# Performance work log

Measured on AMD Instinct MI355X. Metric: run time of the kernel, lower is better.

The kernel has to match this reference:

```python
import jax, jax.numpy as jnp
import numpy as np

N, D, H, O = 200000, 256, 256, 128


def _linear_params(key, fan_in, fan_out):
    # matches torch.nn.Linear default init: U(-1/sqrt(fan_in), 1/sqrt(fan_in))
    lim = 1.0 / np.sqrt(fan_in)
    kw, kb = jax.random.split(key)
    W = jax.random.uniform(kw, (fan_in, fan_out), minval=-lim, maxval=lim, dtype=jnp.float32)
    b = jax.random.uniform(kb, (fan_out,), minval=-lim, maxval=lim, dtype=jnp.float32)
    return W, b


def setup_inputs() -> dict:
    key = jax.random.key(0)
    ks = jax.random.split(key, 6)
    node_embeddings = jax.random.normal(ks[0], (N, D), dtype=jnp.float32)
    # adjacency_list keys: all < N so every key is 'valid'
    adj_keys = jax.random.randint(ks[1], (N,), 0, N, dtype=jnp.int64) if jax.config.jax_enable_x64 else jax.random.randint(ks[1], (N,), 0, N, dtype=jnp.int32)
    W1, b1 = _linear_params(ks[2], D, H)
    W2, b2 = _linear_params(ks[3], H, H)
    W3, b3 = _linear_params(ks[4], H, H)
    Wo, bo = _linear_params(ks[5], H, O)
    return {
        "node_embeddings": node_embeddings,
        "adj_keys": adj_keys,
        "W1": W1, "b1": b1,
        "W2": W2, "b2": b2,
        "W3": W3, "b3": b3,
        "Wo": Wo, "bo": bo,
    }


def reference(node_embeddings, adj_keys, W1, b1, W2, b2, W3, b3, Wo, bo):
    # --- aggregation path (faithful to the torch code's actual math) ---
    # All adj_keys are < N, so valid_indices == keys and the re-enumeration
    # `mapping` makes `indices` exactly arange(num_keys).
    indices = jnp.arange(adj_keys.shape[0])
    neighbors = node_embeddings[indices]              # [N, D] row gather
    # torch.mean(row, dim=0) on a 1-D row == scalar mean over features
    aggregated_embeddings = jnp.mean(neighbors, axis=1)  # [N]

    # --- dense 3-layer SAGE MLP + output projection ---
    x = jax.nn.relu(node_embeddings @ W1 + b1)        # [N, H]
    x = jax.nn.relu(x @ W2 + b2)                      # [N, H]
    x = jax.nn.relu(x @ W3 + b3)                      # [N, H]
    x = x @ Wo + bo                                   # [N, O]
    return (x, aggregated_embeddings)
```

## Files before the change

kernel.cpp:

```cpp
#include <hip/hip_runtime.h>
#include <hip/hip_bf16.h>
#include <cstdint>


#define N_ROWS 200000
#define O_DIM  128
#define ROWS   64
#define PITCH  264

typedef short bf16x8 __attribute__((ext_vector_type(8)));
typedef float f32x4  __attribute__((ext_vector_type(4)));

__device__ __forceinline__ unsigned short rne_bf16(float f) {
  unsigned int u = __float_as_uint(f);
  u += 0x7FFFu + ((u >> 16) & 1u);
  return (unsigned short)(u >> 16);
}

__global__ __launch_bounds__(256) void prep_kernel(
    const float* __restrict__ W1, const float* __restrict__ W2,
    const float* __restrict__ W3, const float* __restrict__ Wo,
    unsigned short* __restrict__ wt) {
  __shared__ float tile[64][65];
  const int b = blockIdx.x;
  int which, tb;
  if (b < 48) { which = b >> 4; tb = b & 15; }
  else        { which = 3;      tb = b - 48; }
  const float* W = (which == 0) ? W1 : (which == 1) ? W2 : (which == 2) ? W3 : Wo;
  const int O = (which == 3) ? 128 : 256;
  unsigned short* out = wt + (size_t)which * 65536;
  const int otiles = O >> 6;
  const int r0 = (tb / otiles) * 64;
  const int c0 = (tb % otiles) * 64;

  const int j  = threadIdx.x & 63;
  const int ib = threadIdx.x >> 6;
#pragma unroll
  for (int ii = 0; ii < 16; ++ii) {
    const int i = ii * 4 + ib;
    tile[i][j] = W[(size_t)(r0 + i) * O + c0 + j];
  }
  __syncthreads();
#pragma unroll
  for (int ii = 0; ii < 16; ++ii) {
    const int i = ii * 4 + ib;
    out[(size_t)(c0 + i) * 256 + r0 + j] = rne_bf16(tile[j][i]);
  }
}

template <int MB, bool RELU, bool LAST>
__device__ __forceinline__ void do_layer(
    const unsigned short* __restrict__ wt, const float* __restrict__ bias,
    float* __restrict__ out_x, long row0, unsigned short* act,
    int wave, int lane) {
  const int lc   = lane & 15;
  const int quad = lane >> 4;
  const int m_base = wave * (MB * 16);
  constexpr int NB = ROWS / 16;

  f32x4 acc[MB][NB];
#pragma unroll
  for (int mb = 0; mb < MB; ++mb)
#pragma unroll
    for (int nb = 0; nb < NB; ++nb)
      acc[mb][nb] = (f32x4){0.f, 0.f, 0.f, 0.f};

#pragma unroll
  for (int k0 = 0; k0 < 256; k0 += 32) {
    bf16x8 bfr[NB];
#pragma unroll
    for (int nb = 0; nb < NB; ++nb)
      bfr[nb] = *(const bf16x8*)&act[(nb * 16 + lc) * PITCH + k0 + 8 * quad];
#pragma unroll
    for (int mb = 0; mb < MB; ++mb) {
      bf16x8 afr = *(const bf16x8*)&wt[(m_base + mb * 16 + lc) * 256 + k0 + 8 * quad];
#pragma unroll
      for (int nb = 0; nb < NB; ++nb)
        acc[mb][nb] = __builtin_amdgcn_mfma_f32_16x16x32_bf16(afr, bfr[nb],
                                                              acc[mb][nb], 0, 0, 0);
    }
  }
  __syncthreads();

#pragma unroll
  for (int mb = 0; mb < MB; ++mb) {
    const int ch = m_base + mb * 16 + 4 * quad;
    f32x4 bb = *(const f32x4*)(bias + ch);
#pragma unroll
    for (int nb = 0; nb < NB; ++nb) {
      f32x4 v = acc[mb][nb] + bb;
      if (RELU) {
#pragma unroll
        for (int j = 0; j < 4; ++j) v[j] = fmaxf(v[j], 0.f);
      }
      const int r = nb * 16 + lc;
      if (!LAST) {
        ushort4 h;
        h.x = rne_bf16(v[0]); h.y = rne_bf16(v[1]);
        h.z = rne_bf16(v[2]); h.w = rne_bf16(v[3]);
        *(ushort4*)&act[r * PITCH + ch] = h;
      } else {
        *(f32x4*)&out_x[(row0 + r) * O_DIM + ch] = v;
      }
    }
  }
  __syncthreads();
}

__global__ __launch_bounds__(256, 4) void sage_kernel(
    const float* __restrict__ E,
    const float* __restrict__ b1, const float* __restrict__ b2,
    const float* __restrict__ b3, const float* __restrict__ bo,
    const unsigned short* __restrict__ wts,
    float* __restrict__ out_x, float* __restrict__ out_agg) {
  __shared__ __align__(16) unsigned short act[ROWS * PITCH];

  const int t    = threadIdx.x;
  const int wave = t >> 6;
  const int lane = t & 63;
  const long row0 = (long)blockIdx.x * ROWS;

#pragma unroll
  for (int i = 0; i < ROWS / 4; ++i) {
    const int r = 4 * i + wave;
    const long gr = row0 + r;
    f32x4 v = *(const f32x4*)(E + gr * 256 + lane * 4);
    ushort4 h;
    h.x = rne_bf16(v[0]); h.y = rne_bf16(v[1]);
    h.z = rne_bf16(v[2]); h.w = rne_bf16(v[3]);
    *(ushort4*)&act[r * PITCH + lane * 4] = h;
    float s = v[0] + v[1] + v[2] + v[3];
    s += __shfl_down(s, 32);
    s += __shfl_down(s, 16);
    s += __shfl_down(s, 8);
    s += __shfl_down(s, 4);
    s += __shfl_down(s, 2);
    s += __shfl_down(s, 1);
    if (lane == 0) out_agg[gr] = s * (1.0f / 256.0f);
  }
  __syncthreads();

  do_layer<4, true,  false>(wts,          b1, nullptr, row0, act, wave, lane);
  do_layer<4, true,  false>(wts + 65536,  b2, nullptr, row0, act, wave, lane);
  do_layer<4, true,  false>(wts + 131072, b3, nullptr, row0, act, wave, lane);
  do_layer<2, false, true >(wts + 196608, bo, out_x,   row0, act, wave, lane);
}

extern "C" void kernel_launch(void* const* d_in, const int* in_sizes, int n_in,
                              void* d_out, int out_size, void* d_ws, size_t ws_size,
                              hipStream_t stream) {
  const float* E  = (const float*)d_in[0];
  const float* W1 = (const float*)d_in[2];
  const float* b1 = (const float*)d_in[3];
  const float* W2 = (const float*)d_in[4];
  const float* b2 = (const float*)d_in[5];
  const float* W3 = (const float*)d_in[6];
  const float* b3 = (const float*)d_in[7];
  const float* Wo = (const float*)d_in[8];
  const float* bo = (const float*)d_in[9];

  float* out_x   = (float*)d_out;
  float* out_agg = out_x + (size_t)N_ROWS * O_DIM;
  unsigned short* wts = (unsigned short*)d_ws;

  prep_kernel<<<56, 256, 0, stream>>>(W1, W2, W3, Wo, wts);

  const int grid = N_ROWS / ROWS;
  sage_kernel<<<grid, 256, 0, stream>>>(E, b1, b2, b3, bo, wts, out_x, out_agg);
}
```

Before: 540.6 us.

## Split fused MLP into per-layer kernels with register-resident weights and global activations

After: 927.4 us. 71.6% more time.

```diff
diff --git a/kernel.cpp b/kernel.cpp
--- a/kernel.cpp
+++ b/kernel.cpp
@@ -4,9 +4,6 @@
 
 
 #define N_ROWS 200000
-#define O_DIM  128
-#define ROWS   64
-#define PITCH  264
 
 typedef short bf16x8 __attribute__((ext_vector_type(8)));
 typedef float f32x4  __attribute__((ext_vector_type(4)));
@@ -15,6 +12,22 @@
   unsigned int u = __float_as_uint(f);
   u += 0x7FFFu + ((u >> 16) & 1u);
   return (unsigned short)(u >> 16);
+}
+
+__device__ __forceinline__ bf16x8 pack8(f32x4 a, f32x4 c) {
+  union { bf16x8 v; __hip_bfloat162 h[4]; } u;
+  u.h[0] = __float22bfloat162_rn(make_float2(a[0], a[1]));
+  u.h[1] = __float22bfloat162_rn(make_float2(a[2], a[3]));
+  u.h[2] = __float22bfloat162_rn(make_float2(c[0], c[1]));
+  u.h[3] = __float22bfloat162_rn(make_float2(c[2], c[3]));
+  return u.v;
+}
+
+__device__ __forceinline__ ushort4 pack4(f32x4 v) {
+  union { ushort4 s; __hip_bfloat162 h[2]; } u;
+  u.h[0] = __float22bfloat162_rn(make_float2(v[0], v[1]));
+  u.h[1] = __float22bfloat162_rn(make_float2(v[2], v[3]));
+  return u.s;
 }
 
 __global__ __launch_bounds__(256) void prep_kernel(
@@ -32,7 +45,6 @@
   const int otiles = O >> 6;
   const int r0 = (tb / otiles) * 64;
   const int c0 = (tb % otiles) * 64;
-
   const int j  = threadIdx.x & 63;
   const int ib = threadIdx.x >> 6;
 #pragma unroll
@@ -48,102 +60,160 @@
   }
 }
 
-template <int MB, bool RELU, bool LAST>
-__device__ __forceinline__ void do_layer(
-    const unsigned short* __restrict__ wt, const float* __restrict__ bias,
-    float* __restrict__ out_x, long row0, unsigned short* act,
-    int wave, int lane) {
-  const int lc   = lane & 15;
-  const int quad = lane >> 4;
-  const int m_base = wave * (MB * 16);
-  constexpr int NB = ROWS / 16;
-
-  f32x4 acc[MB][NB];
-#pragma unroll
-  for (int mb = 0; mb < MB; ++mb)
-#pragma unroll
-    for (int nb = 0; nb < NB; ++nb)
-      acc[mb][nb] = (f32x4){0.f, 0.f, 0.f, 0.f};
-
-#pragma unroll
-  for (int k0 = 0; k0 < 256; k0 += 32) {
-    bf16x8 bfr[NB];
-#pragma unroll
-    for (int nb = 0; nb < NB; ++nb)
-      bfr[nb] = *(const bf16x8*)&act[(nb * 16 + lc) * PITCH + k0 + 8 * quad];
-#pragma unroll
-    for (int mb = 0; mb < MB; ++mb) {
-      bf16x8 afr = *(const bf16x8*)&wt[(m_base + mb * 16 + lc) * 256 + k0 + 8 * quad];
-#pragma unroll
-      for (int nb = 0; nb < NB; ++nb)
-        acc[mb][nb] = __builtin_amdgcn_mfma_f32_16x16x32_bf16(afr, bfr[nb],
-                                                              acc[mb][nb], 0, 0, 0);
+__global__ __launch_bounds__(256, 2) void layer1_kernel(
+    const float* __restrict__ E, const unsigned short* __restrict__ wt,
+    const float* __restrict__ bias, unsigned short* act, float* out_agg) {
+  const int t = threadIdx.x, wave = t >> 6, lane = t & 63;
+  const int lc = lane & 15, quad = lane >> 4;
+  const size_t row0 = (size_t)blockIdx.x * 64;
+  const int m_base = wave * 64;
+  const bool w0 = (wave == 0);
+
+  bf16x8 afr[4][8];
+#pragma unroll
+  for (int mb = 0; mb < 4; ++mb)
+#pragma unroll
+    for (int ks = 0; ks < 8; ++ks)
+      afr[mb][ks] = *(const bf16x8*)&wt[(size_t)(m_base + mb * 16 + lc) * 256 + ks * 32 + 8 * quad];
+
+  f32x4 bb[4];
+#pragma unroll
+  for (int mb = 0; mb < 4; ++mb)
+    bb[mb] = *(const f32x4*)&bias[m_base + mb * 16 + 4 * quad];
+
+  bf16x8 bfr[2][8];
+  float s[2];
+
+#define STAGE1(b, g) do {                                                     \
+    float _sum = 0.f;                                                         \
+    const float* _ep = E + (row0 + (size_t)(g) * 16 + lc) * 256 + 8 * quad;   \
+    _Pragma("unroll")                                                         \
+    for (int ks = 0; ks < 8; ++ks) {                                          \
+      f32x4 _a = *(const f32x4*)(_ep + ks * 32);                              \
+      f32x4 _c = *(const f32x4*)(_ep + ks * 32 + 4);                          \
+      if (w0) _sum += _a[0]+_a[1]+_a[2]+_a[3]+_c[0]+_c[1]+_c[2]+_c[3];        \
+      bfr[b][ks] = pack8(_a, _c);                                             \
+    }                                                                         \
+    s[b] = _sum;                                                              \
+  } while (0)
+
+  STAGE1(0, 0);
+#pragma unroll
+  for (int g = 0; g < 4; ++g) {
+    if (g < 3) STAGE1((g + 1) & 1, g + 1);
+    f32x4 acc[4] = {};
+#pragma unroll
+    for (int ks = 0; ks < 8; ++ks)
+#pragma unroll
+      for (int mb = 0; mb < 4; ++mb)
+        acc[mb] = __builtin_amdgcn_mfma_f32_16x16x32_bf16(afr[mb][ks], bfr[g & 1][ks], acc[mb], 0, 0, 0);
+
+    float sg = s[g & 1];
+    sg += __shfl_xor(sg, 16);
+    sg += __shfl_xor(sg, 32);
+    if (w0 && lane < 16) out_agg[row0 + g * 16 + lane] = sg * (1.0f / 256.0f);
+
+    const size_t r = row0 + g * 16 + lc;
+#pragma unroll
+    for (int mb = 0; mb < 4; ++mb) {
+      f32x4 v = acc[mb] + bb[mb];
+#pragma unroll
+      for (int j = 0; j < 4; ++j) v[j] = fmaxf(v[j], 0.f);
+      *(ushort4*)&act[r * 256 + m_base + mb * 16 + 4 * quad] = pack4(v);
     }
   }
+#undef STAGE1
+}
+
+__global__ __launch_bounds__(256, 2) void layer_mid_kernel(
+    unsigned short* act, const unsigned short* __restrict__ wt,
+    const float* __restrict__ bias) {
+  const int t = threadIdx.x, wave = t >> 6, lane = t & 63;
+  const int lc = lane & 15, quad = lane >> 4;
+  const size_t row0 = (size_t)blockIdx.x * 32;
+  const int m_base = wave * 64;
+
+  bf16x8 bfr[2][8];
+#pragma unroll
+  for (int g = 0; g < 2; ++g)
+#pragma unroll
+    for (int ks = 0; ks < 8; ++ks)
+      bfr[g][ks] = *(const bf16x8*)&act[(row0 + g * 16 + lc) * 256 + ks * 32 + 8 * quad];
+
+  bf16x8 afr[4][8];
+#pragma unroll
+  for (int mb = 0; mb < 4; ++mb)
+#pragma unroll
+    for (int ks = 0; ks < 8; ++ks)
+      afr[mb][ks] = *(const bf16x8*)&wt[(size_t)(m_base + mb * 16 + lc) * 256 + ks * 32 + 8 * quad];
+
+  f32x4 bb[4];
+#pragma unroll
+  for (int mb = 0; mb < 4; ++mb)
+    bb[mb] = *(const f32x4*)&bias[m_base + mb * 16 + 4 * quad];
+
   __syncthreads();
 
 #pragma unroll
-  for (int mb = 0; mb < MB; ++mb) {
-    const int ch = m_base + mb * 16 + 4 * quad;
-    f32x4 bb = *(const f32x4*)(bias + ch);
-#pragma unroll
-    for (int nb = 0; nb < NB; ++nb) {
-      f32x4 v = acc[mb][nb] + bb;
-      if (RELU) {
-#pragma unroll
-        for (int j = 0; j < 4; ++j) v[j] = fmaxf(v[j], 0.f);
-      }
-      const int r = nb * 16 + lc;
-      if (!LAST) {
-        ushort4 h;
-        h.x = rne_bf16(v[0]); h.y = rne_bf16(v[1]);
-        h.z = rne_bf16(v[2]); h.w = rne_bf16(v[3]);
-        *(ushort4*)&act[r * PITCH + ch] = h;
-      } else {
-        *(f32x4*)&out_x[(row0 + r) * O_DIM + ch] = v;
-      }
+  for (int g = 0; g < 2; ++g) {
+    f32x4 acc[4] = {};
+#pragma unroll
+    for (int ks = 0; ks < 8; ++ks)
+#pragma unroll
+      for (int mb = 0; mb < 4; ++mb)
+        acc[mb] = __builtin_amdgcn_mfma_f32_16x16x32_bf16(afr[mb][ks], bfr[g][ks], acc[mb], 0, 0, 0);
+    const size_t r = row0 + g * 16 + lc;
+#pragma unroll
+    for (int mb = 0; mb < 4; ++mb) {
+      f32x4 v = acc[mb] + bb[mb];
+#pragma unroll
+      for (int j = 0; j < 4; ++j) v[j] = fmaxf(v[j], 0.f);
+      *(ushort4*)&act[r * 256 + m_base + mb * 16 + 4 * quad] = pack4(v);
     }
   }
+}
+
+__global__ __launch_bounds__(256, 2) void layer_out_kernel(
+    const unsigned short* actc, float* out_x,
+    const unsigned short* __restrict__ wt, const float* __restrict__ bias) {
+  const int t = threadIdx.x, wave = t >> 6, lane = t & 63;
+  const int lc = lane & 15, quad = lane >> 4;
+  const size_t row0 = (size_t)blockIdx.x * 32;
+  const int m_base = (wave & 1) * 64;
+  const int g = wave >> 1;
+  const size_t r = row0 + g * 16 + lc;
+
+  bf16x8 bfr[8];
+#pragma unroll
+  for (int ks = 0; ks < 8; ++ks)
+    bfr[ks] = *(const bf16x8*)&actc[r * 256 + ks * 32 + 8 * quad];
+
+  bf16x8 afr[4][8];
+#pragma unroll
+  for (int mb = 0; mb < 4; ++mb)
+#pragma unroll
+    for (int ks = 0; ks < 8; ++ks)
+      afr[mb][ks] = *(const bf16x8*)&wt[(size_t)(m_base + mb * 16 + lc) * 256 + ks * 32 + 8 * quad];
+
+  f32x4 bb[4];
+#pragma unroll
+  for (int mb = 0; mb < 4; ++mb)
+    bb[mb] = *(const f32x4*)&bias[m_base + mb * 16 + 4 * quad];
+
   __syncthreads();
-}
-
-__global__ __launch_bounds__(256, 4) void sage_kernel(
-    const float* __restrict__ E,
-    const float* __restrict__ b1, const float* __restrict__ b2,
-    const float* __restrict__ b3, const float* __restrict__ bo,
-    const unsigned short* __restrict__ wts,
-    float* __restrict__ out_x, float* __restrict__ out_agg) {
-  __shared__ __align__(16) unsigned short act[ROWS * PITCH];
-
-  const int t    = threadIdx.x;
-  const int wave = t >> 6;
-  const int lane = t & 63;
-  const long row0 = (long)blockIdx.x * ROWS;
-
-#pragma unroll
-  for (int i = 0; i < ROWS / 4; ++i) {
-    const int r = 4 * i + wave;
-    const long gr = row0 + r;
-    f32x4 v = *(const f32x4*)(E + gr * 256 + lane * 4);
-    ushort4 h;
-    h.x = rne_bf16(v[0]); h.y = rne_bf16(v[1]);
-    h.z = rne_bf16(v[2]); h.w = rne_bf16(v[3]);
-    *(ushort4*)&act[r * PITCH + lane * 4] = h;
-    float s = v[0] + v[1] + v[2] + v[3];
-    s += __shfl_down(s, 32);
-    s += __shfl_down(s, 16);
-    s += __shfl_down(s, 8);
-    s += __shfl_down(s, 4);
-    s += __shfl_down(s, 2);
-    s += __shfl_down(s, 1);
-    if (lane == 0) out_agg[gr] = s * (1.0f / 256.0f);
-  }
-  __syncthreads();
-
-  do_layer<4, true,  false>(wts,          b1, nullptr, row0, act, wave, lane);
-  do_layer<4, true,  false>(wts + 65536,  b2, nullptr, row0, act, wave, lane);
-  do_layer<4, true,  false>(wts + 131072, b3, nullptr, row0, act, wave, lane);
-  do_layer<2, false, true >(wts + 196608, bo, out_x,   row0, act, wave, lane);
+
+  f32x4 acc[4] = {};
+#pragma unroll
+  for (int ks = 0; ks < 8; ++ks)
+#pragma unroll
+    for (int mb = 0; mb < 4; ++mb)
+      acc[mb] = __builtin_amdgcn_mfma_f32_16x16x32_bf16(afr[mb][ks], bfr[ks], acc[mb], 0, 0, 0);
+
+#pragma unroll
+  for (int mb = 0; mb < 4; ++mb) {
+    f32x4 v = acc[mb] + bb[mb];
+    *(f32x4*)&out_x[r * 128 + m_base + mb * 16 + 4 * quad] = v;
+  }
 }
 
 extern "C" void kernel_launch(void* const* d_in, const int* in_sizes, int n_in,
@@ -159,12 +229,14 @@
   const float* Wo = (const float*)d_in[8];
   const float* bo = (const float*)d_in[9];
 
+  unsigned short* wts    = (unsigned short*)d_ws;
+  unsigned short* actbuf = (unsigned short*)d_out;
   float* out_x   = (float*)d_out;
-  float* out_agg = out_x + (size_t)N_ROWS * O_DIM;
-  unsigned short* wts = (unsigned short*)d_ws;
+  float* out_agg = out_x + (size_t)N_ROWS * 128;
 
   prep_kernel<<<56, 256, 0, stream>>>(W1, W2, W3, Wo, wts);
-
-  const int grid = N_ROWS / ROWS;
-  sage_kernel<<<grid, 256, 0, stream>>>(E, b1, b2, b3, bo, wts, out_x, out_agg);
-}
+  layer1_kernel  <<<N_ROWS / 64, 256, 0, stream>>>(E, wts, b1, actbuf, out_agg);
+  layer_mid_kernel<<<N_ROWS / 32, 256, 0, stream>>>(actbuf, wts + 65536,  b2);
+  layer_mid_kernel<<<N_ROWS / 32, 256, 0, stream>>>(actbuf, wts + 131072, b3);
+  layer_out_kernel<<<N_ROWS / 32, 256, 0, stream>>>(actbuf, out_x, wts + 196608, bo);
+}
```
